# Kernel optimization log

Measured on AMD Instinct MI355X. Metric: run time of the kernel, lower is better.

The kernel has to match this reference:

```python
import jax, jax.numpy as jnp
import numpy as np

EPS = 1e-5

@jax.custom_vjp
def ste_quantize(w):
    # abs-mean scale, round, clamp to {-1, 0, 1}
    scale = jnp.maximum(jnp.mean(jnp.abs(w)), EPS)
    return jnp.clip(jnp.round(w / scale), -1.0, 1.0)

def _ste_fwd(w):
    return ste_quantize(w), None

def _ste_bwd(_, g):
    # straight-through: gradient passes unchanged
    return (g,)

ste_quantize.defvjp(_ste_fwd, _ste_bwd)


def setup_inputs() -> dict:
    key = jax.random.key(0)
    k1, k2 = jax.random.split(key)
    x = jax.random.normal(k1, (8, 8192, 1024), dtype=jnp.float32)       # [B, S, in]
    weight = jax.random.normal(k2, (1024, 1024), dtype=jnp.float32) * 0.02  # [out, in]
    return {"x": x, "weight": weight}


def reference(x, weight):
    w_ternary = ste_quantize(weight)                         # [out, in] in {-1,0,1}
    scale = jnp.maximum(jnp.mean(jnp.abs(weight)), EPS)      # scalar (differentiable path)
    # F.linear(x, w_ternary * scale): out = x @ (w_ternary*scale)^T
    return jnp.einsum('bsi,oi->bso', x, w_ternary * scale)
```

## Files before the change

### kernel.cpp

```cpp
#include <hip/hip_runtime.h>
#include <stdint.h>

#define K_DIM 1024
#define N_DIM 1024
#define M_MAX 65536

typedef __attribute__((ext_vector_type(8))) __bf16 bf16x8;
typedef __attribute__((ext_vector_type(4))) float f32x4;

__device__ __align__(16) unsigned short g_wq[N_DIM * K_DIM];
__device__ __align__(16) unsigned short g_xq[(size_t)M_MAX * K_DIM];
__device__ double g_partial[256];
__device__ float g_scale;

__device__ __forceinline__ unsigned int pack_bf16(float hi, float lo) {
  return __builtin_amdgcn_perm(__float_as_uint(hi), __float_as_uint(lo), 0x07060302u);
}

__global__ void absum_kernel(const float* __restrict__ w) {
  const int tid = threadIdx.x, bid = blockIdx.x;
  const float4* w4 = (const float4*)w;
  double s = 0.0;
#pragma unroll
  for (int i = 0; i < 4; i++) {
    float4 v = w4[bid * 1024 + i * 256 + tid];
    s += (double)fabsf(v.x) + (double)fabsf(v.y) + (double)fabsf(v.z) + (double)fabsf(v.w);
  }
#pragma unroll
  for (int o = 32; o > 0; o >>= 1) s += __shfl_down(s, o);
  __shared__ double sm[4];
  if ((tid & 63) == 0) sm[tid >> 6] = s;
  __syncthreads();
  if (tid == 0) g_partial[bid] = sm[0] + sm[1] + sm[2] + sm[3];
}

__global__ void scale_kernel() {
  const int tid = threadIdx.x;
  double v = g_partial[tid];
#pragma unroll
  for (int o = 32; o > 0; o >>= 1) v += __shfl_down(v, o);
  __shared__ double sm[4];
  if ((tid & 63) == 0) sm[tid >> 6] = v;
  __syncthreads();
  if (tid == 0) {
    double total = sm[0] + sm[1] + sm[2] + sm[3];
    double mean = total * (1.0 / 1048576.0);
    g_scale = (float)fmax(mean, 1e-5);
  }
}

__global__ void quant_kernel(const float* __restrict__ w) {
  const int idx = blockIdx.x * 256 + threadIdx.x;
  const float s = g_scale;
  float4 v = ((const float4*)w)[idx];
  float q0 = fminf(1.f, fmaxf(-1.f, rintf(v.x / s)));
  float q1 = fminf(1.f, fmaxf(-1.f, rintf(v.y / s)));
  float q2 = fminf(1.f, fmaxf(-1.f, rintf(v.z / s)));
  float q3 = fminf(1.f, fmaxf(-1.f, rintf(v.w / s)));
  ushort4 o;
  o.x = (unsigned short)(__float_as_uint(q0) >> 16);
  o.y = (unsigned short)(__float_as_uint(q1) >> 16);
  o.z = (unsigned short)(__float_as_uint(q2) >> 16);
  o.w = (unsigned short)(__float_as_uint(q3) >> 16);
  ((ushort4*)g_wq)[idx] = o;
}

__global__ __launch_bounds__(256) void convert_x(const float* __restrict__ x) {
  const size_t t = (size_t)blockIdx.x * 256 + threadIdx.x;
  const float4* x4 = (const float4*)x;
  float4 a = x4[t * 2];
  float4 b = x4[t * 2 + 1];
  uint4 o;
  o.x = pack_bf16(a.y, a.x);
  o.y = pack_bf16(a.w, a.z);
  o.z = pack_bf16(b.y, b.x);
  o.w = pack_bf16(b.w, b.z);
  ((uint4*)g_xq)[t] = o;
}

__global__ __launch_bounds__(256) void bitlinear_gemm(float* __restrict__ C) {
  __shared__ __align__(16) unsigned short As[128 * 32];
  __shared__ __align__(16) unsigned short Bs[128 * 32];

  const int tid  = threadIdx.x;
  const int lane = tid & 63;
  const int wave = tid >> 6;
  const int wm   = (wave >> 1) * 64;
  const int wn   = (wave & 1) * 64;
  const int lm   = lane & 15;
  const int lq   = lane >> 4;

  const int b  = blockIdx.x;
  const int mt = (b >> 6) * 8 + (b & 7);
  const int nt = (b >> 3) & 7;
  const int m0 = mt * 128;
  const int n0 = nt * 128;

  f32x4 acc[4][4];
#pragma unroll
  for (int i = 0; i < 4; i++)
#pragma unroll
    for (int j = 0; j < 4; j++) acc[i][j] = (f32x4){0.f, 0.f, 0.f, 0.f};

  const unsigned short* aptr =
      g_xq + (size_t)(m0 + wave * 32 + (lane >> 2)) * K_DIM + (lane & 3) * 8;
  const unsigned short* bptr =
      g_wq + (size_t)(n0 + wave * 32 + (lane >> 2)) * K_DIM + (lane & 3) * 8;

  for (int kc = 0; kc < K_DIM; kc += 32) {
    __builtin_amdgcn_global_load_lds(
        (const __attribute__((address_space(1))) unsigned int*)(aptr + kc),
        (__attribute__((address_space(3))) unsigned int*)&As[(wave * 32) * 32],
        16, 0, 0);
    __builtin_amdgcn_global_load_lds(
        (const __attribute__((address_space(1))) unsigned int*)(aptr + 16 * K_DIM + kc),
        (__attribute__((address_space(3))) unsigned int*)&As[(wave * 32 + 16) * 32],
        16, 0, 0);
    __builtin_amdgcn_global_load_lds(
        (const __attribute__((address_space(1))) unsigned int*)(bptr + kc),
        (__attribute__((address_space(3))) unsigned int*)&Bs[(wave * 32) * 32],
        16, 0, 0);
    __builtin_amdgcn_global_load_lds(
        (const __attribute__((address_space(1))) unsigned int*)(bptr + 16 * K_DIM + kc),
        (__attribute__((address_space(3))) unsigned int*)&Bs[(wave * 32 + 16) * 32],
        16, 0, 0);

    __syncthreads();

    const bf16x8* Ap = (const bf16x8*)&As[(wm + lm) * 32 + lq * 8];
    const bf16x8* Bp = (const bf16x8*)&Bs[(wn + lm) * 32 + lq * 8];
    bf16x8 af[4], bfr[4];
#pragma unroll
    for (int t = 0; t < 4; t++) {
      af[t]  = Ap[t * 64];
      bfr[t] = Bp[t * 64];
    }
#pragma unroll
    for (int i = 0; i < 4; i++)
#pragma unroll
      for (int j = 0; j < 4; j++)
        acc[i][j] =
            __builtin_amdgcn_mfma_f32_16x16x32_bf16(af[i], bfr[j], acc[i][j], 0, 0, 0);

    __syncthreads();
  }

  const float s = g_scale;
#pragma unroll
  for (int i = 0; i < 4; i++) {
#pragma unroll
    for (int j = 0; j < 4; j++) {
#pragma unroll
      for (int r = 0; r < 4; r++) {
        const int row = m0 + wm + i * 16 + lq * 4 + r;
        const int col = n0 + wn + j * 16 + lm;
        C[(size_t)row * N_DIM + col] = acc[i][j][r] * s;
      }
    }
  }
}

extern "C" void kernel_launch(void* const* d_in, const int* in_sizes, int n_in,
                              void* d_out, int out_size, void* d_ws, size_t ws_size,
                              hipStream_t stream) {
  const float* x = (const float*)d_in[0];
  const float* w = (const float*)d_in[1];
  float* out = (float*)d_out;
  const int M = in_sizes[0] / K_DIM;

  hipLaunchKernelGGL(absum_kernel, dim3(256), dim3(256), 0, stream, w);
  hipLaunchKernelGGL(scale_kernel, dim3(1), dim3(256), 0, stream);
  hipLaunchKernelGGL(quant_kernel, dim3(1024), dim3(256), 0, stream, w);
  hipLaunchKernelGGL(convert_x, dim3((unsigned)((size_t)M * K_DIM / 8 / 256)), dim3(256), 0,
                     stream, x);
  hipLaunchKernelGGL(bitlinear_gemm, dim3((unsigned)(((size_t)M / 128) * (N_DIM / 128))),
                     dim3(256), 0, stream, out);
}
```

Before: 671.1 us.

## Rewrite GEMM with 256x256 tiles, triple-buffered LDS and swizzled reads

```diff
diff --git a/kernel.cpp b/kernel.cpp
--- a/kernel.cpp
+++ b/kernel.cpp
@@ -4,6 +4,14 @@
 #define K_DIM 1024
 #define N_DIM 1024
 #define M_MAX 65536
+
+#define BM 256
+#define BN 256
+#define BK 32
+#define NKT (K_DIM / BK)
+#define NBUF 3
+#define A_TILE (BM * BK)
+#define B_TILE (BN * BK)
 
 typedef __attribute__((ext_vector_type(8))) __bf16 bf16x8;
 typedef __attribute__((ext_vector_type(4))) float f32x4;
@@ -78,83 +86,133 @@
   ((uint4*)g_xq)[t] = o;
 }
 
-__global__ __launch_bounds__(256) void bitlinear_gemm(float* __restrict__ C) {
-  __shared__ __align__(16) unsigned short As[128 * 32];
-  __shared__ __align__(16) unsigned short Bs[128 * 32];
+__global__ __launch_bounds__(512, 2) void bitlinear_gemm(float* __restrict__ C) {
+  __shared__ __align__(16) unsigned short As[NBUF * A_TILE];
+  __shared__ __align__(16) unsigned short Bs[NBUF * B_TILE];
 
   const int tid  = threadIdx.x;
   const int lane = tid & 63;
   const int wave = tid >> 6;
-  const int wm   = (wave >> 1) * 64;
-  const int wn   = (wave & 1) * 64;
+  const int wm   = wave >> 2;
+  const int wn   = wave & 3;
   const int lm   = lane & 15;
   const int lq   = lane >> 4;
 
-  const int b  = blockIdx.x;
-  const int mt = (b >> 6) * 8 + (b & 7);
-  const int nt = (b >> 3) & 7;
-  const int m0 = mt * 128;
-  const int n0 = nt * 128;
-
-  f32x4 acc[4][4];
-#pragma unroll
-  for (int i = 0; i < 4; i++)
+  const int b       = blockIdx.x;
+  const int cpx     = (int)(gridDim.x >> 3);
+  const int logical = (b & 7) * cpx + (b >> 3);
+  const int mt      = logical >> 2;
+  const int nt      = logical & 3;
+  const int m0      = mt * BM;
+  const int n0      = nt * BN;
+
+  f32x4 acc[8][4];
+#pragma unroll
+  for (int i = 0; i < 8; i++)
 #pragma unroll
     for (int j = 0; j < 4; j++) acc[i][j] = (f32x4){0.f, 0.f, 0.f, 0.f};
 
-  const unsigned short* aptr =
-      g_xq + (size_t)(m0 + wave * 32 + (lane >> 2)) * K_DIM + (lane & 3) * 8;
-  const unsigned short* bptr =
-      g_wq + (size_t)(n0 + wave * 32 + (lane >> 2)) * K_DIM + (lane & 3) * 8;
-
-  for (int kc = 0; kc < K_DIM; kc += 32) {
-    __builtin_amdgcn_global_load_lds(
-        (const __attribute__((address_space(1))) unsigned int*)(aptr + kc),
-        (__attribute__((address_space(3))) unsigned int*)&As[(wave * 32) * 32],
-        16, 0, 0);
-    __builtin_amdgcn_global_load_lds(
-        (const __attribute__((address_space(1))) unsigned int*)(aptr + 16 * K_DIM + kc),
-        (__attribute__((address_space(3))) unsigned int*)&As[(wave * 32 + 16) * 32],
-        16, 0, 0);
-    __builtin_amdgcn_global_load_lds(
-        (const __attribute__((address_space(1))) unsigned int*)(bptr + kc),
-        (__attribute__((address_space(3))) unsigned int*)&Bs[(wave * 32) * 32],
-        16, 0, 0);
-    __builtin_amdgcn_global_load_lds(
-        (const __attribute__((address_space(1))) unsigned int*)(bptr + 16 * K_DIM + kc),
-        (__attribute__((address_space(3))) unsigned int*)&Bs[(wave * 32 + 16) * 32],
-        16, 0, 0);
-
-    __syncthreads();
-
-    const bf16x8* Ap = (const bf16x8*)&As[(wm + lm) * 32 + lq * 8];
-    const bf16x8* Bp = (const bf16x8*)&Bs[(wn + lm) * 32 + lq * 8];
-    bf16x8 af[4], bfr[4];
-#pragma unroll
-    for (int t = 0; t < 4; t++) {
-      af[t]  = Ap[t * 64];
-      bfr[t] = Bp[t * 64];
-    }
-#pragma unroll
-    for (int i = 0; i < 4; i++)
-#pragma unroll
-      for (int j = 0; j < 4; j++)
-        acc[i][j] =
-            __builtin_amdgcn_mfma_f32_16x16x32_bf16(af[i], bfr[j], acc[i][j], 0, 0, 0);
-
-    __syncthreads();
-  }
-
-  const float s = g_scale;
-#pragma unroll
-  for (int i = 0; i < 4; i++) {
-#pragma unroll
-    for (int j = 0; j < 4; j++) {
-#pragma unroll
-      for (int r = 0; r < 4; r++) {
-        const int row = m0 + wm + i * 16 + lq * 4 + r;
-        const int col = n0 + wn + j * 16 + lm;
-        C[(size_t)row * N_DIM + col] = acc[i][j][r] * s;
+  const int cswz = ((lane & 3) ^ ((lane >> 3) & 3)) * 8;
+  const unsigned short* aSrc =
+      g_xq + (size_t)(m0 + wave * 32 + (lane >> 2)) * K_DIM + cswz;
+  const unsigned short* bSrc =
+      g_wq + (size_t)(n0 + wave * 32 + (lane >> 2)) * K_DIM + cswz;
+  const int ldsDst = wave * 32 * BK;
+
+#define STAGE_A(tt, bb)                                                        \
+  do {                                                                         \
+    const unsigned short* s_ = aSrc + (tt) * BK;                               \
+    unsigned short* d_ = &As[(bb) * A_TILE + ldsDst];                          \
+    __builtin_amdgcn_global_load_lds(                                          \
+        (const __attribute__((address_space(1))) unsigned int*)s_,             \
+        (__attribute__((address_space(3))) unsigned int*)d_, 16, 0, 0);        \
+    __builtin_amdgcn_global_load_lds(                                          \
+        (const __attribute__((address_space(1))) unsigned int*)(s_ + 16 * K_DIM), \
+        (__attribute__((address_space(3))) unsigned int*)(d_ + 16 * BK), 16, 0, 0); \
+  } while (0)
+
+#define STAGE_B(tt, bb)                                                        \
+  do {                                                                         \
+    const unsigned short* s_ = bSrc + (tt) * BK;                               \
+    unsigned short* d_ = &Bs[(bb) * B_TILE + ldsDst];                          \
+    __builtin_amdgcn_global_load_lds(                                          \
+        (const __attribute__((address_space(1))) unsigned int*)s_,             \
+        (__attribute__((address_space(3))) unsigned int*)d_, 16, 0, 0);        \
+    __builtin_amdgcn_global_load_lds(                                          \
+        (const __attribute__((address_space(1))) unsigned int*)(s_ + 16 * K_DIM), \
+        (__attribute__((address_space(3))) unsigned int*)(d_ + 16 * BK), 16, 0, 0); \
+  } while (0)
+
+  const int xorc = (((lm >> 1) & 3) ^ lq) * 8;
+  const int aRd  = (wm * 128 + lm) * BK + xorc;
+  const int bRd  = (wn * 64 + lm) * BK + xorc;
+
+  STAGE_A(0, 0);
+  STAGE_B(0, 0);
+  STAGE_A(1, 1);
+  STAGE_B(1, 1);
+
+  int buf = 0;
+#pragma unroll 1
+  for (int t = 0; t < NKT; ++t) {
+    if (t == NKT - 1)
+      asm volatile("s_waitcnt vmcnt(0)\n\ts_barrier" ::: "memory");
+    else
+      asm volatile("s_waitcnt vmcnt(4)\n\ts_barrier" ::: "memory");
+
+    const unsigned short* Ab = &As[buf * A_TILE + aRd];
+    const unsigned short* Bb = &Bs[buf * B_TILE + bRd];
+    const int nbuf = (buf + 2 >= NBUF) ? buf + 2 - NBUF : buf + 2;
+
+    bf16x8 bfr[4], af[4];
+#pragma unroll
+    for (int nf = 0; nf < 4; ++nf) bfr[nf] = *(const bf16x8*)(Bb + nf * 16 * BK);
+#pragma unroll
+    for (int mf = 0; mf < 4; ++mf) af[mf] = *(const bf16x8*)(Ab + mf * 16 * BK);
+
+    if (t + 2 < NKT) STAGE_A(t + 2, nbuf);
+
+    __builtin_amdgcn_s_setprio(1);
+#pragma unroll
+    for (int mf = 0; mf < 4; ++mf)
+#pragma unroll
+      for (int nf = 0; nf < 4; ++nf)
+        acc[mf][nf] = __builtin_amdgcn_mfma_f32_16x16x32_bf16(af[mf], bfr[nf],
+                                                              acc[mf][nf], 0, 0, 0);
+    __builtin_amdgcn_s_setprio(0);
+
+    bf16x8 af2[4];
+#pragma unroll
+    for (int mf = 0; mf < 4; ++mf)
+      af2[mf] = *(const bf16x8*)(Ab + (mf + 4) * 16 * BK);
+
+    if (t + 2 < NKT) STAGE_B(t + 2, nbuf);
+
+    __builtin_amdgcn_s_setprio(1);
+#pragma unroll
+    for (int mf = 0; mf < 4; ++mf)
+#pragma unroll
+      for (int nf = 0; nf < 4; ++nf)
+        acc[mf + 4][nf] = __builtin_amdgcn_mfma_f32_16x16x32_bf16(
+            af2[mf], bfr[nf], acc[mf + 4][nf], 0, 0, 0);
+    __builtin_amdgcn_s_setprio(0);
+
+    buf = (buf + 1 == NBUF) ? 0 : buf + 1;
+  }
+#undef STAGE_A
+#undef STAGE_B
+
+  const float s    = g_scale;
+  const int   crow = m0 + wm * 128 + lq * 4;
+  const int   ccol = n0 + wn * 64 + lm;
+#pragma unroll
+  for (int mf = 0; mf < 8; ++mf) {
+#pragma unroll
+    for (int nf = 0; nf < 4; ++nf) {
+#pragma unroll
+      for (int r = 0; r < 4; ++r) {
+        C[(size_t)(crow + mf * 16 + r) * N_DIM + (ccol + nf * 16)] =
+            acc[mf][nf][r] * s;
       }
     }
   }
@@ -173,6 +231,7 @@
   hipLaunchKernelGGL(quant_kernel, dim3(1024), dim3(256), 0, stream, w);
   hipLaunchKernelGGL(convert_x, dim3((unsigned)((size_t)M * K_DIM / 8 / 256)), dim3(256), 0,
                      stream, x);
-  hipLaunchKernelGGL(bitlinear_gemm, dim3((unsigned)(((size_t)M / 128) * (N_DIM / 128))),
-                     dim3(256), 0, stream, out);
-}
+  hipLaunchKernelGGL(bitlinear_gemm,
+                     dim3((unsigned)(((size_t)M / BM) * (N_DIM / BN))),
+                     dim3(512), 0, stream, out);
+}
```

Result: faster. 620.0 us (-7.6%).
